# Performance work log

Hardware: AMD Instinct MI355X
Metric: run time of the kernel (lower is better)

## Reference

```python
import jax, jax.numpy as jnp
import numpy as np

N = 100000       # nodes
E = 1600000      # edges
IN = 256         # in_channels
H = 64           # hidden_channels
OUT = 40         # out_channels
K = 3            # hops

def setup_inputs() -> dict:
    key = jax.random.key(0)
    ks = jax.random.split(key, 20)
    f = lambda k, s: jax.random.normal(k, s, dtype=jnp.float32) * 0.05
    return {
        'x': f(ks[0], (N, IN)),
        'edge_index': jax.random.randint(ks[1], (2, E), 0, N),
        'W_in': f(ks[2], (H, IN)), 'b_in': f(ks[3], (H,)),
        'sg_W': f(ks[4], (K, H, H)), 'sg_b': f(ks[5], (K, H)),
        'in_proj_W': f(ks[6], (3 * H, H)), 'in_proj_b': f(ks[7], (3 * H,)),
        'out_W': f(ks[8], (H, H)), 'out_b': f(ks[9], (H,)),
        'ff_W1': f(ks[10], (2 * H, H)), 'ff_b1': f(ks[11], (2 * H,)),
        'ff_W2': f(ks[12], (H, 2 * H)), 'ff_b2': f(ks[13], (H,)),
        'ln1_w': jnp.ones((H,), jnp.float32), 'ln1_b': jnp.zeros((H,), jnp.float32),
        'ln2_w': jnp.ones((H,), jnp.float32), 'ln2_b': jnp.zeros((H,), jnp.float32),
        'cls_W': f(ks[14], (OUT, H)), 'cls_b': f(ks[15], (OUT,)),
    }

def _ln(x, w, b, eps=1e-5):
    m = x.mean(-1, keepdims=True)
    v = ((x - m) ** 2).mean(-1, keepdims=True)
    return (x - m) * jax.lax.rsqrt(v + eps) * w + b

def reference(x, edge_index, W_in, b_in, sg_W, sg_b, in_proj_W, in_proj_b,
              out_W, out_b, ff_W1, ff_b1, ff_W2, ff_b2,
              ln1_w, ln1_b, ln2_w, ln2_b, cls_W, cls_b):
    # --- gcn_norm with self loops (SGConv default) ---
    loop = jnp.arange(N)
    src = jnp.concatenate([edge_index[0], loop])
    dst = jnp.concatenate([edge_index[1], loop])
    deg = jax.ops.segment_sum(jnp.ones(src.shape[0], x.dtype), dst, num_segments=N)
    dinv = jnp.where(deg > 0, jax.lax.rsqrt(deg), 0.0)
    norm = dinv[src] * dinv[dst]  # [E+N]

    def prop(h):  # one symmetric-normalized propagation: S @ h
        return jax.ops.segment_sum(h[src] * norm[:, None], dst, num_segments=N)

    h0 = jax.nn.relu(x @ W_in.T + b_in)  # [N, H]
    # SGConv with K=hop recomputes S^hop h0; equivalently propagate iteratively
    tokens = [h0]
    p = h0
    for k in range(K):
        p = prop(p)
        tokens.append(jax.nn.relu(p @ sg_W[k].T + sg_b[k]))
    seq = jnp.stack(tokens, axis=1)  # [N, K+1, H]

    # --- TransformerEncoderLayer (nhead=1, post-norm, gelu), eval mode ---
    qkv = seq @ in_proj_W.T + in_proj_b
    q, kk, v = jnp.split(qkv, 3, axis=-1)
    scores = jnp.einsum('nsh,nth->nst', q, kk) / jnp.sqrt(jnp.asarray(H, seq.dtype))
    a = jnp.einsum('nst,nth->nsh', jax.nn.softmax(scores, axis=-1), v)
    a = a @ out_W.T + out_b
    seq = _ln(seq + a, ln1_w, ln1_b)
    ff = jax.nn.gelu(seq @ ff_W1.T + ff_b1, approximate=False) @ ff_W2.T + ff_b2
    seq = _ln(seq + ff, ln2_w, ln2_b)

    h = seq.mean(axis=1)  # [N, H]
    return h @ cls_W.T + cls_b  # [N, OUT]
```

## Files before the change

### kernel.cpp

```cpp
#include <hip/hip_runtime.h>
#include <hip/hip_bf16.h>
#include <math.h>

#define NN 100000
#define EE 1600000
#define OUTC 40
#define NB 391
#define NG 6250
#define CAP 64
#define NBIN 391
#define BCAP 6144

#define WP_WIN 0
#define WP_SG  16896
#define WP_QKV 30720
#define WP_WO  44544
#define WP_W1  49152
#define WP_W2  58368
#define WP_WC  67072
#define WP_TOT 70528

typedef __hip_bfloat16 bf16;
typedef __attribute__((ext_vector_type(8))) short bf16x8;
typedef __attribute__((ext_vector_type(4))) float f32x4;

__device__ __forceinline__ unsigned short f2us(float f){
  bf16 b = __float2bfloat16(f);
  unsigned short u; __builtin_memcpy(&u, &b, 2); return u;
}
__device__ __forceinline__ float us2f(unsigned short u){
  union{unsigned x; float f;} c; c.x = ((unsigned)u)<<16; return c.f;
}
__device__ __forceinline__ float lo_f(unsigned u){ union{unsigned x;float f;}c; c.x = u<<16; return c.f; }
__device__ __forceinline__ float hi_f(unsigned u){ union{unsigned x;float f;}c; c.x = u & 0xffff0000u; return c.f; }

__device__ __forceinline__ float gelu_f(float v){
  float ax = fabsf(v);
  float t  = __builtin_amdgcn_rcpf(fmaf(0.3275911f, ax, 1.0f));
  float p  = fmaf(t, 1.061405429f, -1.453152027f);
  p = fmaf(t, p, 1.421413741f);
  p = fmaf(t, p, -0.284496736f);
  p = fmaf(t, p, 0.254829592f);
  p = p * t;
  float ex = __expf(-ax*ax);
  float er = fmaf(-p, ex, 1.0f);
  er = copysignf(er, v);
  return 0.5f * v * (1.0f + er);
}

__global__ void k_wprep(const float* __restrict__ Win, const float* __restrict__ sgW,
                        const float* __restrict__ Wqkv, const float* __restrict__ Wo,
                        const float* __restrict__ W1, const float* __restrict__ W2,
                        const float* __restrict__ Wc, unsigned short* __restrict__ wp){
  for (int idx = blockIdx.x*blockDim.x + threadIdx.x; idx < WP_TOT;
       idx += gridDim.x*blockDim.x){
    float v; int o;
    if (idx < WP_SG){ o = idx; int r=o/264, c=o-r*264; v = (c<256)? Win[r*256+c] : 0.f; }
    else if (idx < WP_QKV){ o = idx-WP_SG; int h=o/4608, rem=o-h*4608, r=rem/72, c=rem-r*72;
      v=(c<64)? sgW[h*4096+r*64+c] : 0.f; }
    else if (idx < WP_WO){ o = idx-WP_QKV; int r=o/72, c=o-r*72; v=(c<64)? Wqkv[r*64+c]:0.f; }
    else if (idx < WP_W1){ o = idx-WP_WO; int r=o/72, c=o-r*72; v=(c<64)? Wo[r*64+c]:0.f; }
    else if (idx < WP_W2){ o = idx-WP_W1; int r=o/72, c=o-r*72; v=(c<64)? W1[r*64+c]:0.f; }
    else if (idx < WP_WC){ o = idx-WP_W2; int r=o/136, c=o-r*136; v=(c<128)? W2[r*128+c]:0.f; }
    else { o = idx-WP_WC; int r=o/72, c=o-r*72; v=(r<OUTC && c<64)? Wc[r*64+c]:0.f; }
    wp[idx] = f2us(v);
  }
}

__global__ void k_zero(int* p, int n){
  int i = blockIdx.x*blockDim.x + threadIdx.x;
  if (i < n) p[i] = 0;
}

__global__ void __launch_bounds__(256) k_bin(const int* __restrict__ ei,
    int* __restrict__ binFill, int2* __restrict__ binned){
  __shared__ int hist[NBIN], sbase[NBIN], loc[NBIN];
  const int tid = threadIdx.x;
  const int CH = (EE + gridDim.x - 1) / gridDim.x;
  const int e0 = blockIdx.x * CH;
  const int e1 = min(e0 + CH, EE);
  for (int i = tid; i < NBIN; i += 256){ hist[i] = 0; loc[i] = 0; }
  __syncthreads();
  for (int e = e0 + tid; e < e1; e += 256)
    atomicAdd(&hist[ei[EE + e] >> 8], 1);
  __syncthreads();
  for (int i = tid; i < NBIN; i += 256)
    sbase[i] = atomicAdd(&binFill[i], hist[i]);
  __syncthreads();
  for (int e = e0 + tid; e < e1; e += 256){
    int d = ei[EE + e];
    int s = ei[e];
    int b = d >> 8;
    int p = sbase[b] + atomicAdd(&loc[b], 1);
    if (p < BCAP) binned[(size_t)b*BCAP + p] = make_int2(s, d);
  }
}
__global__ void __launch_bounds__(256) k_bucket(const int* __restrict__ binFill,
    const int2* __restrict__ binned, int* __restrict__ srcb,
    int* __restrict__ cnt, float* __restrict__ dinv){
  __shared__ int lcnt[256];
  const int b = blockIdx.x, tid = threadIdx.x;
  lcnt[tid] = 0;
  __syncthreads();
  int m = binFill[b]; if (m > BCAP) m = BCAP;
  const int2* seg = binned + (size_t)b*BCAP;
  for (int e = tid; e < m; e += 256){
    int2 sd = seg[e];
    int dl = sd.y & 255;
    int p = atomicAdd(&lcnt[dl], 1);
    if (p < CAP) srcb[((size_t)(b << 8) + dl)*CAP + p] = sd.x;
  }
  __syncthreads();
  int d = (b << 8) + tid;
  if (d < NN){
    int c = lcnt[tid];
    dinv[d] = rsqrtf((float)c + 1.0f);
    cnt[d] = min(c, CAP);
  }
}

__global__ void __launch_bounds__(256) k_gather(const int* __restrict__ cnt,
    const int* __restrict__ srcb, const float* __restrict__ dinv,
    const unsigned short* __restrict__ prev, unsigned short* __restrict__ cur){
  int wid = (blockIdx.x*256 + threadIdx.x) >> 6;
  if (wid >= NN) return;
  const int lane = threadIdx.x & 63;
  const int grp = lane >> 4, cl = lane & 15;
  const int n = wid;
  const int deg = cnt[n];
  const int* bk = srcb + (size_t)n*CAP;
  const float dn = dinv[n];
  float a0=0.f, a1=0.f, a2=0.f, a3=0.f;
  int base = 0;
  if (8 <= deg){
    int s0 = bk[grp], s1 = bk[4+grp];
    float w0 = dinv[s0]*dn, w1 = dinv[s1]*dn;
    uint2 r0 = *(const uint2*)(prev + ((size_t)s0 << 6) + (cl << 2));
    uint2 r1 = *(const uint2*)(prev + ((size_t)s1 << 6) + (cl << 2));
    base = 8;
    for (; base + 8 <= deg; base += 8){
      int t0 = bk[base + grp], t1 = bk[base + 4 + grp];
      float x0 = dinv[t0]*dn, x1 = dinv[t1]*dn;
      uint2 q0 = *(const uint2*)(prev + ((size_t)t0 << 6) + (cl << 2));
      uint2 q1 = *(const uint2*)(prev + ((size_t)t1 << 6) + (cl << 2));
      a0 += lo_f(r0.x)*w0; a1 += hi_f(r0.x)*w0;
      a2 += lo_f(r0.y)*w0; a3 += hi_f(r0.y)*w0;
      a0 += lo_f(r1.x)*w1; a1 += hi_f(r1.x)*w1;
      a2 += lo_f(r1.y)*w1; a3 += hi_f(r1.y)*w1;
      s0 = t0; s1 = t1; w0 = x0; w1 = x1; r0 = q0; r1 = q1;
    }
    a0 += lo_f(r0.x)*w0; a1 += hi_f(r0.x)*w0;
    a2 += lo_f(r0.y)*w0; a3 += hi_f(r0.y)*w0;
    a0 += lo_f(r1.x)*w1; a1 += hi_f(r1.x)*w1;
    a2 += lo_f(r1.y)*w1; a3 += hi_f(r1.y)*w1;
  }
  for (; base < deg; base += 4){
    int idx = base + grp;
    int s = 0; float w = 0.f;
    if (idx < deg){ s = bk[idx]; w = dinv[s]*dn; }
    uint2 r0 = *(const uint2*)(prev + ((size_t)s << 6) + (cl << 2));
    a0 += lo_f(r0.x)*w; a1 += hi_f(r0.x)*w;
    a2 += lo_f(r0.y)*w; a3 += hi_f(r0.y)*w;
  }
  a0 += __shfl_xor(a0,16); a0 += __shfl_xor(a0,32);
  a1 += __shfl_xor(a1,16); a1 += __shfl_xor(a1,32);
  a2 += __shfl_xor(a2,16); a2 += __shfl_xor(a2,32);
  a3 += __shfl_xor(a3,16); a3 += __shfl_xor(a3,32);
  if (lane < 16){
    float d2 = dn*dn;
    uint2 sr = *(const uint2*)(prev + ((size_t)n << 6) + (cl << 2));
    a0 += lo_f(sr.x)*d2; a1 += hi_f(sr.x)*d2;
    a2 += lo_f(sr.y)*d2; a3 += hi_f(sr.y)*d2;
    unsigned p0 = (unsigned)f2us(a0) | ((unsigned)f2us(a1) << 16);
    unsigned p1 = (unsigned)f2us(a2) | ((unsigned)f2us(a3) << 16);
    *(uint2*)(cur + ((size_t)n << 6) + (cl << 2)) = make_uint2(p0, p1);
  }
}

__global__ void __launch_bounds__(256) k_h0(const float* __restrict__ x,
    const unsigned short* __restrict__ wp, const float* __restrict__ bin,
    unsigned short* __restrict__ tokB, unsigned short* __restrict__ p0){
  __shared__ __align__(16) unsigned short Xs[64*264];
  __shared__ __align__(16) unsigned short Ws[64*264];
  __shared__ float bs[64];
  const int tid = threadIdx.x;
  {
    const uint4* src = (const uint4*)(wp + WP_WIN);
    for (int idx = tid; idx < 2112; idx += 256) ((uint4*)Ws)[idx] = src[idx];
  }
  const int n0 = blockIdx.x * 64;
  for (int idx = tid; idx < 4096; idx += 256){
    int r = idx >> 6, c0 = (idx & 63) * 4;
    int n = n0 + r; if (n >= NN) n = NN-1;
    float4 v = *(const float4*)(x + (size_t)n*256 + c0);
    unsigned short* d = &Xs[r*264 + c0];
    d[0]=f2us(v.x); d[1]=f2us(v.y); d[2]=f2us(v.z); d[3]=f2us(v.w);
  }
  if (tid < 64) bs[tid] = bin[tid];
  __syncthreads();
  const int w = tid >> 6, lane = tid & 63, quad = lane >> 4, c = lane & 15;
  f32x4 acc[4] = {{0,0,0,0},{0,0,0,0},{0,0,0,0},{0,0,0,0}};
  #pragma unroll
  for (int ks = 0; ks < 8; ++ks){
    int k0 = ks*32 + quad*8;
    bf16x8 a = *(const bf16x8*)&Xs[(w*16 + c)*264 + k0];
    #pragma unroll
    for (int nt = 0; nt < 4; ++nt){
      bf16x8 b = *(const bf16x8*)&Ws[(nt*16 + c)*264 + k0];
      acc[nt] = __builtin_amdgcn_mfma_f32_16x16x32_bf16(a, b, acc[nt], 0,0,0);
    }
  }
  __syncthreads();
  #pragma unroll
  for (int nt = 0; nt < 4; ++nt){
    int col = nt*16 + c;
    float bb = bs[col];
    #pragma unroll
    for (int rg = 0; rg < 4; ++rg){
      int rloc = w*16 + quad*4 + rg;
      Xs[rloc*72 + col] = f2us(fmaxf(acc[nt][rg] + bb, 0.f));
    }
  }
  __syncthreads();
  for (int idx = tid; idx < 512; idx += 256){
    int r = idx >> 3, ch = idx & 7;
    int n = n0 + r;
    if (n < NN){
      uint4 v = *(const uint4*)&Xs[r*72 + ch*8];
      *(uint4*)(tokB + (size_t)n*64 + ch*8) = v;
      *(uint4*)(p0   + (size_t)n*64 + ch*8) = v;
    }
  }
}

__global__ void __launch_bounds__(256) k_token(const unsigned short* __restrict__ cur,
    const unsigned short* __restrict__ wsg, const float* __restrict__ sgb,
    unsigned short* __restrict__ tok){
  __shared__ __align__(16) unsigned short Xs[64*72];
  __shared__ __align__(16) unsigned short Ws[64*72];
  __shared__ float bs[64];
  const int tid = threadIdx.x;
  {
    const uint4* src = (const uint4*)wsg;
    for (int idx = tid; idx < 576; idx += 256) ((uint4*)Ws)[idx] = src[idx];
  }
  if (tid < 64) bs[tid] = sgb[tid];
  const int n0 = blockIdx.x*64;
  for (int idx = tid; idx < 512; idx += 256){
    int r = idx >> 3, ch = idx & 7;
    int n = n0 + r; if (n >= NN) n = NN-1;
    *(uint4*)&Xs[r*72 + ch*8] = *(const uint4*)(cur + (size_t)n*64 + ch*8);
  }
  __syncthreads();
  const int w = tid >> 6, lane = tid & 63, quad = lane >> 4, c = lane & 15;
  f32x4 acc[4] = {{0,0,0,0},{0,0,0,0},{0,0,0,0},{0,0,0,0}};
  #pragma unroll
  for (int ks = 0; ks < 2; ++ks){
    int k0 = ks*32 + quad*8;
    bf16x8 a = *(const bf16x8*)&Xs[(w*16 + c)*72 + k0];
    #pragma unroll
    for (int nt = 0; nt < 4; ++nt){
      bf16x8 b = *(const bf16x8*)&Ws[(nt*16 + c)*72 + k0];
      acc[nt] = __builtin_amdgcn_mfma_f32_16x16x32_bf16(a, b, acc[nt], 0,0,0);
    }
  }
  __syncthreads();
  #pragma unroll
  for (int nt = 0; nt < 4; ++nt){
    int col = nt*16 + c;
    float bb = bs[col];
    #pragma unroll
    for (int rg = 0; rg < 4; ++rg){
      int rloc = w*16 + quad*4 + rg;
      Xs[rloc*72 + col] = f2us(fmaxf(acc[nt][rg] + bb, 0.f));
    }
  }
  __syncthreads();
  for (int idx = tid; idx < 512; idx += 256){
    int r = idx >> 3, ch = idx & 7;
    int n = n0 + r;
    if (n < NN)
      *(uint4*)(tok + (size_t)n*64 + ch*8) = *(const uint4*)&Xs[r*72 + ch*8];
  }
}

__global__ void __launch_bounds__(256) k_attn(unsigned short* __restrict__ tokB,
    const unsigned short* __restrict__ wp, const float* __restrict__ bqkv,
    const float* __restrict__ bo, const float* __restrict__ ln1w,
    const float* __restrict__ ln1b){
  __shared__ __align__(16) unsigned short Xs[64*72];
  __shared__ float bq[192], bos[64], l1w[64], l1b[64];
  const int tid = threadIdx.x;
  if (tid < 192) bq[tid] = bqkv[tid];
  if (tid < 64){ bos[tid]=bo[tid]; l1w[tid]=ln1w[tid]; l1b[tid]=ln1b[tid]; }
  const int w = tid >> 6, lane = tid & 63, quad = lane >> 4, c = lane & 15;
  const int rw = w*16;
  const unsigned short* Wq  = wp + WP_QKV;
  const unsigned short* Wos = wp + WP_WO;
  for (int g = blockIdx.x; g < NG; g += gridDim.x){
    __syncthreads();
    for (int idx = tid; idx < 512; idx += 256){
      int r = idx >> 3, ch = idx & 7;
      int t = r & 3, n = g*16 + (r >> 2);
      *(uint4*)&Xs[r*72 + ch*8] = *(const uint4*)(tokB + ((size_t)t*NN + n)*64 + ch*8);
    }
    __syncthreads();
    bf16x8 a0 = *(const bf16x8*)&Xs[(rw+c)*72 + quad*8];
    bf16x8 a1 = *(const bf16x8*)&Xs[(rw+c)*72 + 32 + quad*8];
    float resv[4][4];
    #pragma unroll
    for (int nt = 0; nt < 4; ++nt){
      #pragma unroll
      for (int rg = 0; rg < 4; ++rg)
        resv[nt][rg] = us2f(Xs[(rw + quad*4 + rg)*72 + nt*16 + c]);
    }
    f32x4 qk[12];
    #pragma unroll
    for (int nt = 0; nt < 12; ++nt){
      f32x4 acc = {0,0,0,0};
      bf16x8 b0 = *(const bf16x8*)&Wq[(nt*16+c)*72 + quad*8];
      bf16x8 b1 = *(const bf16x8*)&Wq[(nt*16+c)*72 + 32 + quad*8];
      acc = __builtin_amdgcn_mfma_f32_16x16x32_bf16(a0, b0, acc, 0,0,0);
      acc = __builtin_amdgcn_mfma_f32_16x16x32_bf16(a1, b1, acc, 0,0,0);
      float bb = bq[nt*16 + c];
      acc[0]+=bb; acc[1]+=bb; acc[2]+=bb; acc[3]+=bb;
      qk[nt] = acc;
    }
    float sc[4][4];
    #pragma unroll
    for (int s = 0; s < 4; ++s){
      #pragma unroll
      for (int t = 0; t < 4; ++t){
        float p = qk[0][s]*qk[4][t] + qk[1][s]*qk[5][t]
                + qk[2][s]*qk[6][t] + qk[3][s]*qk[7][t];
        p += __shfl_xor(p, 1); p += __shfl_xor(p, 2);
        p += __shfl_xor(p, 4); p += __shfl_xor(p, 8);
        sc[s][t] = p * 0.125f;
      }
    }
    float pm[4][4];
    #pragma unroll
    for (int s = 0; s < 4; ++s){
      float m = fmaxf(fmaxf(sc[s][0],sc[s][1]), fmaxf(sc[s][2],sc[s][3]));
      float e0=__expf(sc[s][0]-m), e1=__expf(sc[s][1]-m);
      float e2=__expf(sc[s][2]-m), e3=__expf(sc[s][3]-m);
      float inv = 1.f/(e0+e1+e2+e3);
      pm[s][0]=e0*inv; pm[s][1]=e1*inv; pm[s][2]=e2*inv; pm[s][3]=e3*inv;
    }
    #pragma unroll
    for (int tile = 0; tile < 4; ++tile){
      #pragma unroll
      for (int s = 0; s < 4; ++s){
        float av = pm[s][0]*qk[8+tile][0] + pm[s][1]*qk[8+tile][1]
                 + pm[s][2]*qk[8+tile][2] + pm[s][3]*qk[8+tile][3];
        Xs[(rw + quad*4 + s)*72 + tile*16 + c] = f2us(av);
      }
    }
    bf16x8 p0 = *(const bf16x8*)&Xs[(rw+c)*72 + quad*8];
    bf16x8 p1 = *(const bf16x8*)&Xs[(rw+c)*72 + 32 + quad*8];
    f32x4 ov[4];
    #pragma unroll
    for (int nt = 0; nt < 4; ++nt){
      f32x4 acc = {0,0,0,0};
      bf16x8 b0 = *(const bf16x8*)&Wos[(nt*16+c)*72 + quad*8];
      bf16x8 b1 = *(const bf16x8*)&Wos[(nt*16+c)*72 + 32 + quad*8];
      acc = __builtin_amdgcn_mfma_f32_16x16x32_bf16(p0, b0, acc, 0,0,0);
      acc = __builtin_amdgcn_mfma_f32_16x16x32_bf16(p1, b1, acc, 0,0,0);
      ov[nt] = acc;
    }
    float r4[4][4];
    #pragma unroll
    for (int nt = 0; nt < 4; ++nt){
      int col = nt*16 + c;
      float bb = bos[col];
      #pragma unroll
      for (int rg = 0; rg < 4; ++rg)
        r4[nt][rg] = ov[nt][rg] + bb + resv[nt][rg];
    }
    #pragma unroll
    for (int rg = 0; rg < 4; ++rg){
      float sm = r4[0][rg]+r4[1][rg]+r4[2][rg]+r4[3][rg];
      sm += __shfl_xor(sm,1); sm += __shfl_xor(sm,2);
      sm += __shfl_xor(sm,4); sm += __shfl_xor(sm,8);
      float mean = sm * (1.f/64.f);
      float d0=r4[0][rg]-mean, d1=r4[1][rg]-mean, d2=r4[2][rg]-mean, d3=r4[3][rg]-mean;
      float vs = d0*d0+d1*d1+d2*d2+d3*d3;
      vs += __shfl_xor(vs,1); vs += __shfl_xor(vs,2);
      vs += __shfl_xor(vs,4); vs += __shfl_xor(vs,8);
      float rinv = rsqrtf(vs*(1.f/64.f) + 1e-5f);
      int row = rw + quad*4 + rg;
      #pragma unroll
      for (int nt = 0; nt < 4; ++nt){
        int col = nt*16 + c;
        Xs[row*72 + col] = f2us((r4[nt][rg] - mean) * rinv * l1w[col] + l1b[col]);
      }
    }
    __syncthreads();
    for (int idx = tid; idx < 512; idx += 256){
      int r = idx >> 3, ch = idx & 7;
      int t = r & 3, n = g*16 + (r >> 2);
      *(uint4*)(tokB + ((size_t)t*NN + n)*64 + ch*8) = *(const uint4*)&Xs[r*72 + ch*8];
    }
  }
}

__global__ void __launch_bounds__(256) k_ffn(const unsigned short* __restrict__ tokB,
    const unsigned short* __restrict__ wp,
    const float* __restrict__ b1, const float* __restrict__ b2,
    const float* __restrict__ ln2w, const float* __restrict__ ln2b,
    const float* __restrict__ bc, float* __restrict__ out){
  __shared__ __align__(16) unsigned short Xs[64*72];
  __shared__ __align__(16) unsigned short F1[64*136];
  __shared__ __align__(16) unsigned short hsH[16*72];
  __shared__ __align__(16) unsigned short hsL[16*72];
  __shared__ float b1s[128], b2s[64], l2w[64], l2b[64], bcs[40];
  const int tid = threadIdx.x;
  if (tid < 128) b1s[tid] = b1[tid];
  if (tid < 64){ b2s[tid]=b2[tid]; l2w[tid]=ln2w[tid]; l2b[tid]=ln2b[tid]; }
  if (tid < 40)  bcs[tid] = bc[tid];
  const int w = tid >> 6, lane = tid & 63, quad = lane >> 4, c = lane & 15;
  const int rw = w*16;
  const unsigned short* W1g = wp + WP_W1;
  const unsigned short* W2g = wp + WP_W2;
  const unsigned short* Wcg = wp + WP_WC;
  for (int g = blockIdx.x; g < NG; g += gridDim.x){
    __syncthreads();
    for (int idx = tid; idx < 512; idx += 256){
      int r = idx >> 3, ch = idx & 7;
      int t = r & 3, n = g*16 + (r >> 2);
      *(uint4*)&Xs[r*72 + ch*8] = *(const uint4*)(tokB + ((size_t)t*NN + n)*64 + ch*8);
    }
    __syncthreads();
    bf16x8 a0 = *(const bf16x8*)&Xs[(rw+c)*72 + quad*8];
    bf16x8 a1 = *(const bf16x8*)&Xs[(rw+c)*72 + 32 + quad*8];
    #pragma unroll
    for (int nt = 0; nt < 8; ++nt){
      f32x4 acc = {0,0,0,0};
      bf16x8 b0 = *(const bf16x8*)&W1g[(nt*16+c)*72 + quad*8];
      bf16x8 b1v = *(const bf16x8*)&W1g[(nt*16+c)*72 + 32 + quad*8];
      acc = __builtin_amdgcn_mfma_f32_16x16x32_bf16(a0, b0, acc, 0,0,0);
      acc = __builtin_amdgcn_mfma_f32_16x16x32_bf16(a1, b1v, acc, 0,0,0);
      float bb = b1s[nt*16 + c];
      #pragma unroll
      for (int rg = 0; rg < 4; ++rg){
        float v = acc[rg] + bb;
        F1[(rw + quad*4 + rg)*136 + nt*16 + c] = f2us(gelu_f(v));
      }
    }
    bf16x8 fa[4];
    #pragma unroll
    for (int ks = 0; ks < 4; ++ks)
      fa[ks] = *(const bf16x8*)&F1[(rw+c)*136 + ks*32 + quad*8];
    f32x4 ov[4];
    #pragma unroll
    for (int nt = 0; nt < 4; ++nt){
      f32x4 acc = {0,0,0,0};
      #pragma unroll
      for (int ks = 0; ks < 4; ++ks){
        bf16x8 b = *(const bf16x8*)&W2g[(nt*16+c)*136 + ks*32 + quad*8];
        acc = __builtin_amdgcn_mfma_f32_16x16x32_bf16(fa[ks], b, acc, 0,0,0);
      }
      ov[nt] = acc;
    }
    float r4[4][4];
    #pragma unroll
    for (int nt = 0; nt < 4; ++nt){
      int col = nt*16 + c;
      float bb = b2s[col];
      #pragma unroll
      for (int rg = 0; rg < 4; ++rg){
        float seqv = us2f(Xs[(rw + quad*4 + rg)*72 + col]);
        r4[nt][rg] = ov[nt][rg] + bb + seqv;
      }
    }
    float hval[4] = {0.f, 0.f, 0.f, 0.f};
    #pragma unroll
    for (int rg = 0; rg < 4; ++rg){
      float sm = r4[0][rg]+r4[1][rg]+r4[2][rg]+r4[3][rg];
      sm += __shfl_xor(sm,1); sm += __shfl_xor(sm,2);
      sm += __shfl_xor(sm,4); sm += __shfl_xor(sm,8);
      float mean = sm * (1.f/64.f);
      float d0=r4[0][rg]-mean, d1=r4[1][rg]-mean, d2=r4[2][rg]-mean, d3=r4[3][rg]-mean;
      float vs = d0*d0+d1*d1+d2*d2+d3*d3;
      vs += __shfl_xor(vs,1); vs += __shfl_xor(vs,2);
      vs += __shfl_xor(vs,4); vs += __shfl_xor(vs,8);
      float rinv = rsqrtf(vs*(1.f/64.f) + 1e-5f);
      #pragma unroll
      for (int nt = 0; nt < 4; ++nt){
        int col = nt*16 + c;
        hval[nt] += (r4[nt][rg] - mean) * rinv * l2w[col] + l2b[col];
      }
    }
    #pragma unroll
    for (int nt = 0; nt < 4; ++nt){
      float hv = hval[nt] * 0.25f;
      unsigned short hh = f2us(hv);
      float lo = hv - us2f(hh);
      hsH[(w*4 + quad)*72 + nt*16 + c] = hh;
      hsL[(w*4 + quad)*72 + nt*16 + c] = f2us(lo);
    }
    __syncthreads();
    if (w < 3){
      bf16x8 hA0 = *(const bf16x8*)&hsH[c*72 + quad*8];
      bf16x8 hA1 = *(const bf16x8*)&hsH[c*72 + 32 + quad*8];
      bf16x8 lA0 = *(const bf16x8*)&hsL[c*72 + quad*8];
      bf16x8 lA1 = *(const bf16x8*)&hsL[c*72 + 32 + quad*8];
      bf16x8 wB0 = *(const bf16x8*)&Wcg[(w*16 + c)*72 + quad*8];
      bf16x8 wB1 = *(const bf16x8*)&Wcg[(w*16 + c)*72 + 32 + quad*8];
      f32x4 acc = {0,0,0,0};
      acc = __builtin_amdgcn_mfma_f32_16x16x32_bf16(hA0, wB0, acc, 0,0,0);
      acc = __builtin_amdgcn_mfma_f32_16x16x32_bf16(hA1, wB1, acc, 0,0,0);
      acc = __builtin_amdgcn_mfma_f32_16x16x32_bf16(lA0, wB0, acc, 0,0,0);
      acc = __builtin_amdgcn_mfma_f32_16x16x32_bf16(lA1, wB1, acc, 0,0,0);
      int o = w*16 + c;
      if (o < OUTC){
        float bb = bcs[o];
        #pragma unroll
        for (int rg = 0; rg < 4; ++rg)
          out[(size_t)(g*16 + quad*4 + rg)*OUTC + o] = acc[rg] + bb;
      }
    }
  }
}

extern "C" void kernel_launch(void* const* d_in, const int* in_sizes, int n_in,
                              void* d_out, int out_size, void* d_ws, size_t ws_size,
                              hipStream_t stream) {
  const float* x    = (const float*)d_in[0];
  const int*   ei   = (const int*  )d_in[1];
  const float* Win  = (const float*)d_in[2];
  const float* bin  = (const float*)d_in[3];
  const float* sgW  = (const float*)d_in[4];
  const float* sgb  = (const float*)d_in[5];
  const float* Wqkv = (const float*)d_in[6];
  const float* bqkv = (const float*)d_in[7];
  const float* Wo   = (const float*)d_in[8];
  const float* bo   = (const float*)d_in[9];
  const float* W1   = (const float*)d_in[10];
  const float* b1   = (const float*)d_in[11];
  const float* W2   = (const float*)d_in[12];
  const float* b2   = (const float*)d_in[13];
  const float* ln1w = (const float*)d_in[14];
  const float* ln1b = (const float*)d_in[15];
  const float* ln2w = (const float*)d_in[16];
  const float* ln2b = (const float*)d_in[17];
  const float* Wc   = (const float*)d_in[18];
  const float* bc   = (const float*)d_in[19];

  char* ws = (char*)d_ws;
  float*          dinv = (float*)(ws);
  int*            cnt  = (int*  )(ws + 400128);
  unsigned short* wp   = (unsigned short*)(ws + 800256);
  unsigned short* tokB = (unsigned short*)(ws + 941568);
  unsigned short* pb0  = (unsigned short*)(ws + 52141696);
  unsigned short* pb1  = (unsigned short*)(ws + 64941824);
  int2* binned  = (int2*)pb0;
  int*  binFill = (int*)tokB;
  int*  srcb    = (int*)(tokB + (size_t)2*NN*64);

  k_wprep<<<128, 256, 0, stream>>>(Win, sgW, Wqkv, Wo, W1, W2, Wc, wp);

  k_zero  <<<2, 256, 0, stream>>>(binFill, NBIN);
  k_bin   <<<512, 256, 0, stream>>>(ei, binFill, binned);
  k_bucket<<<NBIN, 256, 0, stream>>>(binFill, binned, srcb, cnt, dinv);

  const int GB = (NN + 63) / 64;
  const int GG = (NN*64 + 255) / 256;
  k_h0<<<GB, 256, 0, stream>>>(x, wp, bin, tokB, pb0);

  k_gather<<<GG, 256, 0, stream>>>(cnt, srcb, dinv, pb0, pb1);
  k_token <<<GB, 256, 0, stream>>>(pb1, wp + WP_SG,        sgb,       tokB + (size_t)1*NN*64);
  k_gather<<<GG, 256, 0, stream>>>(cnt, srcb, dinv, pb1, pb0);
  k_gather<<<GG, 256, 0, stream>>>(cnt, srcb, dinv, pb0, pb1);
  k_token <<<GB, 256, 0, stream>>>(pb0, wp + WP_SG + 4608, sgb + 64,  tokB + (size_t)2*NN*64);
  k_token <<<GB, 256, 0, stream>>>(pb1, wp + WP_SG + 9216, sgb + 128, tokB + (size_t)3*NN*64);

  k_attn<<<2048, 256, 0, stream>>>(tokB, wp, bqkv, bo, ln1w, ln1b);
  k_ffn <<<2048, 256, 0, stream>>>(tokB, wp, b1, b2, ln2w, ln2b, bc, (float*)d_out);
}
```

Before: 608.4 us.

## Fuse attention and FFN kernels; widen gather loads to 16 bytes per lane

Merges the attention and FFN kernels into one kernel that keeps the LN1 output in shared memory instead of writing it to tokB and reading it back, which removes one global round trip of the token tensor. The attention output now goes to the F1 buffer so Xs can still supply the residual. Separately, the gather kernel now has each lane load 8 bf16 values (uint4) across 8 lanes per row, processing 8 or 16 edges per step. The cost is a larger shared-memory footprint per block, more registers in the fused kernel, and more shuffle steps in the gather reduction.

```diff
diff --git a/kernel.cpp b/kernel.cpp
--- a/kernel.cpp
+++ b/kernel.cpp
@@ -119,61 +119,66 @@
   }
 }
 
+#define GACC(r, wt) \
+  a0 += lo_f((r).x)*(wt); a1 += hi_f((r).x)*(wt); \
+  a2 += lo_f((r).y)*(wt); a3 += hi_f((r).y)*(wt); \
+  a4 += lo_f((r).z)*(wt); a5 += hi_f((r).z)*(wt); \
+  a6 += lo_f((r).w)*(wt); a7 += hi_f((r).w)*(wt);
+
 __global__ void __launch_bounds__(256) k_gather(const int* __restrict__ cnt,
     const int* __restrict__ srcb, const float* __restrict__ dinv,
     const unsigned short* __restrict__ prev, unsigned short* __restrict__ cur){
   int wid = (blockIdx.x*256 + threadIdx.x) >> 6;
   if (wid >= NN) return;
   const int lane = threadIdx.x & 63;
-  const int grp = lane >> 4, cl = lane & 15;
+  const int grp = lane >> 3, cl = lane & 7;
   const int n = wid;
   const int deg = cnt[n];
   const int* bk = srcb + (size_t)n*CAP;
   const float dn = dinv[n];
-  float a0=0.f, a1=0.f, a2=0.f, a3=0.f;
+  float a0=0,a1=0,a2=0,a3=0,a4=0,a5=0,a6=0,a7=0;
   int base = 0;
-  if (8 <= deg){
-    int s0 = bk[grp], s1 = bk[4+grp];
+  if (16 <= deg){
+    int s0 = bk[grp], s1 = bk[8 + grp];
     float w0 = dinv[s0]*dn, w1 = dinv[s1]*dn;
-    uint2 r0 = *(const uint2*)(prev + ((size_t)s0 << 6) + (cl << 2));
-    uint2 r1 = *(const uint2*)(prev + ((size_t)s1 << 6) + (cl << 2));
-    base = 8;
-    for (; base + 8 <= deg; base += 8){
-      int t0 = bk[base + grp], t1 = bk[base + 4 + grp];
+    uint4 r0 = *(const uint4*)(prev + ((size_t)s0 << 6) + (cl << 3));
+    uint4 r1 = *(const uint4*)(prev + ((size_t)s1 << 6) + (cl << 3));
+    base = 16;
+    for (; base + 16 <= deg; base += 16){
+      int t0 = bk[base + grp], t1 = bk[base + 8 + grp];
       float x0 = dinv[t0]*dn, x1 = dinv[t1]*dn;
-      uint2 q0 = *(const uint2*)(prev + ((size_t)t0 << 6) + (cl << 2));
-      uint2 q1 = *(const uint2*)(prev + ((size_t)t1 << 6) + (cl << 2));
-      a0 += lo_f(r0.x)*w0; a1 += hi_f(r0.x)*w0;
-      a2 += lo_f(r0.y)*w0; a3 += hi_f(r0.y)*w0;
-      a0 += lo_f(r1.x)*w1; a1 += hi_f(r1.x)*w1;
-      a2 += lo_f(r1.y)*w1; a3 += hi_f(r1.y)*w1;
+      uint4 q0 = *(const uint4*)(prev + ((size_t)t0 << 6) + (cl << 3));
+      uint4 q1 = *(const uint4*)(prev + ((size_t)t1 << 6) + (cl << 3));
+      GACC(r0, w0); GACC(r1, w1);
       s0 = t0; s1 = t1; w0 = x0; w1 = x1; r0 = q0; r1 = q1;
     }
-    a0 += lo_f(r0.x)*w0; a1 += hi_f(r0.x)*w0;
-    a2 += lo_f(r0.y)*w0; a3 += hi_f(r0.y)*w0;
-    a0 += lo_f(r1.x)*w1; a1 += hi_f(r1.x)*w1;
-    a2 += lo_f(r1.y)*w1; a3 += hi_f(r1.y)*w1;
-  }
-  for (; base < deg; base += 4){
+    GACC(r0, w0); GACC(r1, w1);
+  }
+  for (; base < deg; base += 8){
     int idx = base + grp;
-    int s = 0; float w = 0.f;
-    if (idx < deg){ s = bk[idx]; w = dinv[s]*dn; }
-    uint2 r0 = *(const uint2*)(prev + ((size_t)s << 6) + (cl << 2));
-    a0 += lo_f(r0.x)*w; a1 += hi_f(r0.x)*w;
-    a2 += lo_f(r0.y)*w; a3 += hi_f(r0.y)*w;
-  }
-  a0 += __shfl_xor(a0,16); a0 += __shfl_xor(a0,32);
-  a1 += __shfl_xor(a1,16); a1 += __shfl_xor(a1,32);
-  a2 += __shfl_xor(a2,16); a2 += __shfl_xor(a2,32);
-  a3 += __shfl_xor(a3,16); a3 += __shfl_xor(a3,32);
-  if (lane < 16){
+    int s = 0; float wv = 0.f;
+    if (idx < deg){ s = bk[idx]; wv = dinv[s]*dn; }
+    uint4 r = *(const uint4*)(prev + ((size_t)s << 6) + (cl << 3));
+    GACC(r, wv);
+  }
+  a0 += __shfl_xor(a0,8); a0 += __shfl_xor(a0,16); a0 += __shfl_xor(a0,32);
+  a1 += __shfl_xor(a1,8); a1 += __shfl_xor(a1,16); a1 += __shfl_xor(a1,32);
+  a2 += __shfl_xor(a2,8); a2 += __shfl_xor(a2,16); a2 += __shfl_xor(a2,32);
+  a3 += __shfl_xor(a3,8); a3 += __shfl_xor(a3,16); a3 += __shfl_xor(a3,32);
+  a4 += __shfl_xor(a4,8); a4 += __shfl_xor(a4,16); a4 += __shfl_xor(a4,32);
+  a5 += __shfl_xor(a5,8); a5 += __shfl_xor(a5,16); a5 += __shfl_xor(a5,32);
+  a6 += __shfl_xor(a6,8); a6 += __shfl_xor(a6,16); a6 += __shfl_xor(a6,32);
+  a7 += __shfl_xor(a7,8); a7 += __shfl_xor(a7,16); a7 += __shfl_xor(a7,32);
+  if (lane < 8){
     float d2 = dn*dn;
-    uint2 sr = *(const uint2*)(prev + ((size_t)n << 6) + (cl << 2));
-    a0 += lo_f(sr.x)*d2; a1 += hi_f(sr.x)*d2;
-    a2 += lo_f(sr.y)*d2; a3 += hi_f(sr.y)*d2;
-    unsigned p0 = (unsigned)f2us(a0) | ((unsigned)f2us(a1) << 16);
-    unsigned p1 = (unsigned)f2us(a2) | ((unsigned)f2us(a3) << 16);
-    *(uint2*)(cur + ((size_t)n << 6) + (cl << 2)) = make_uint2(p0, p1);
+    uint4 sr = *(const uint4*)(prev + ((size_t)n << 6) + (cl << 3));
+    GACC(sr, d2);
+    uint4 pk;
+    pk.x = (unsigned)f2us(a0) | ((unsigned)f2us(a1) << 16);
+    pk.y = (unsigned)f2us(a2) | ((unsigned)f2us(a3) << 16);
+    pk.z = (unsigned)f2us(a4) | ((unsigned)f2us(a5) << 16);
+    pk.w = (unsigned)f2us(a6) | ((unsigned)f2us(a7) << 16);
+    *(uint4*)(cur + ((size_t)n << 6) + (cl << 3)) = pk;
   }
 }
 
@@ -284,19 +289,32 @@
   }
 }
 
-__global__ void __launch_bounds__(256) k_attn(unsigned short* __restrict__ tokB,
+__global__ void __launch_bounds__(256) k_attn_ffn(const unsigned short* __restrict__ tokB,
     const unsigned short* __restrict__ wp, const float* __restrict__ bqkv,
     const float* __restrict__ bo, const float* __restrict__ ln1w,
-    const float* __restrict__ ln1b){
+    const float* __restrict__ ln1b,
+    const float* __restrict__ b1, const float* __restrict__ b2,
+    const float* __restrict__ ln2w, const float* __restrict__ ln2b,
+    const float* __restrict__ bc, float* __restrict__ out){
   __shared__ __align__(16) unsigned short Xs[64*72];
+  __shared__ __align__(16) unsigned short F1[64*136];
+  __shared__ __align__(16) unsigned short hsH[16*72];
+  __shared__ __align__(16) unsigned short hsL[16*72];
   __shared__ float bq[192], bos[64], l1w[64], l1b[64];
+  __shared__ float b1s[128], b2s[64], l2w[64], l2b[64], bcs[40];
   const int tid = threadIdx.x;
   if (tid < 192) bq[tid] = bqkv[tid];
-  if (tid < 64){ bos[tid]=bo[tid]; l1w[tid]=ln1w[tid]; l1b[tid]=ln1b[tid]; }
+  if (tid < 128) b1s[tid] = b1[tid];
+  if (tid < 64){ bos[tid]=bo[tid]; l1w[tid]=ln1w[tid]; l1b[tid]=ln1b[tid];
+                 b2s[tid]=b2[tid]; l2w[tid]=ln2w[tid]; l2b[tid]=ln2b[tid]; }
+  if (tid < 40)  bcs[tid] = bc[tid];
   const int w = tid >> 6, lane = tid & 63, quad = lane >> 4, c = lane & 15;
   const int rw = w*16;
   const unsigned short* Wq  = wp + WP_QKV;
   const unsigned short* Wos = wp + WP_WO;
+  const unsigned short* W1g = wp + WP_W1;
+  const unsigned short* W2g = wp + WP_W2;
+  const unsigned short* Wcg = wp + WP_WC;
   for (int g = blockIdx.x; g < NG; g += gridDim.x){
     __syncthreads();
     for (int idx = tid; idx < 512; idx += 256){
@@ -307,21 +325,14 @@
     __syncthreads();
     bf16x8 a0 = *(const bf16x8*)&Xs[(rw+c)*72 + quad*8];
     bf16x8 a1 = *(const bf16x8*)&Xs[(rw+c)*72 + 32 + quad*8];
-    float resv[4][4];
-    #pragma unroll
-    for (int nt = 0; nt < 4; ++nt){
-      #pragma unroll
-      for (int rg = 0; rg < 4; ++rg)
-        resv[nt][rg] = us2f(Xs[(rw + quad*4 + rg)*72 + nt*16 + c]);
-    }
     f32x4 qk[12];
     #pragma unroll
     for (int nt = 0; nt < 12; ++nt){
       f32x4 acc = {0,0,0,0};
       bf16x8 b0 = *(const bf16x8*)&Wq[(nt*16+c)*72 + quad*8];
-      bf16x8 b1 = *(const bf16x8*)&Wq[(nt*16+c)*72 + 32 + quad*8];
+      bf16x8 b1v = *(const bf16x8*)&Wq[(nt*16+c)*72 + 32 + quad*8];
       acc = __builtin_amdgcn_mfma_f32_16x16x32_bf16(a0, b0, acc, 0,0,0);
-      acc = __builtin_amdgcn_mfma_f32_16x16x32_bf16(a1, b1, acc, 0,0,0);
+      acc = __builtin_amdgcn_mfma_f32_16x16x32_bf16(a1, b1v, acc, 0,0,0);
       float bb = bq[nt*16 + c];
       acc[0]+=bb; acc[1]+=bb; acc[2]+=bb; acc[3]+=bb;
       qk[nt] = acc;
@@ -353,19 +364,19 @@
       for (int s = 0; s < 4; ++s){
         float av = pm[s][0]*qk[8+tile][0] + pm[s][1]*qk[8+tile][1]
                  + pm[s][2]*qk[8+tile][2] + pm[s][3]*qk[8+tile][3];
-        Xs[(rw + quad*4 + s)*72 + tile*16 + c] = f2us(av);
-      }
-    }
-    bf16x8 p0 = *(const bf16x8*)&Xs[(rw+c)*72 + quad*8];
-    bf16x8 p1 = *(const bf16x8*)&Xs[(rw+c)*72 + 32 + quad*8];
+        F1[(rw + quad*4 + s)*72 + tile*16 + c] = f2us(av);
+      }
+    }
+    bf16x8 p0 = *(const bf16x8*)&F1[(rw+c)*72 + quad*8];
+    bf16x8 p1 = *(const bf16x8*)&F1[(rw+c)*72 + 32 + quad*8];
     f32x4 ov[4];
     #pragma unroll
     for (int nt = 0; nt < 4; ++nt){
       f32x4 acc = {0,0,0,0};
       bf16x8 b0 = *(const bf16x8*)&Wos[(nt*16+c)*72 + quad*8];
-      bf16x8 b1 = *(const bf16x8*)&Wos[(nt*16+c)*72 + 32 + quad*8];
+      bf16x8 b1v = *(const bf16x8*)&Wos[(nt*16+c)*72 + 32 + quad*8];
       acc = __builtin_amdgcn_mfma_f32_16x16x32_bf16(p0, b0, acc, 0,0,0);
-      acc = __builtin_amdgcn_mfma_f32_16x16x32_bf16(p1, b1, acc, 0,0,0);
+      acc = __builtin_amdgcn_mfma_f32_16x16x32_bf16(p1, b1v, acc, 0,0,0);
       ov[nt] = acc;
     }
     float r4[4][4];
@@ -374,8 +385,10 @@
       int col = nt*16 + c;
       float bb = bos[col];
       #pragma unroll
-      for (int rg = 0; rg < 4; ++rg)
-        r4[nt][rg] = ov[nt][rg] + bb + resv[nt][rg];
+      for (int rg = 0; rg < 4; ++rg){
+        float seqv = us2f(Xs[(rw + quad*4 + rg)*72 + col]);
+        r4[nt][rg] = ov[nt][rg] + bb + seqv;
+      }
     }
     #pragma unroll
     for (int rg = 0; rg < 4; ++rg){
@@ -395,51 +408,15 @@
         Xs[row*72 + col] = f2us((r4[nt][rg] - mean) * rinv * l1w[col] + l1b[col]);
       }
     }
-    __syncthreads();
-    for (int idx = tid; idx < 512; idx += 256){
-      int r = idx >> 3, ch = idx & 7;
-      int t = r & 3, n = g*16 + (r >> 2);
-      *(uint4*)(tokB + ((size_t)t*NN + n)*64 + ch*8) = *(const uint4*)&Xs[r*72 + ch*8];
-    }
-  }
-}
-
-__global__ void __launch_bounds__(256) k_ffn(const unsigned short* __restrict__ tokB,
-    const unsigned short* __restrict__ wp,
-    const float* __restrict__ b1, const float* __restrict__ b2,
-    const float* __restrict__ ln2w, const float* __restrict__ ln2b,
-    const float* __restrict__ bc, float* __restrict__ out){
-  __shared__ __align__(16) unsigned short Xs[64*72];
-  __shared__ __align__(16) unsigned short F1[64*136];
-  __shared__ __align__(16) unsigned short hsH[16*72];
-  __shared__ __align__(16) unsigned short hsL[16*72];
-  __shared__ float b1s[128], b2s[64], l2w[64], l2b[64], bcs[40];
-  const int tid = threadIdx.x;
-  if (tid < 128) b1s[tid] = b1[tid];
-  if (tid < 64){ b2s[tid]=b2[tid]; l2w[tid]=ln2w[tid]; l2b[tid]=ln2b[tid]; }
-  if (tid < 40)  bcs[tid] = bc[tid];
-  const int w = tid >> 6, lane = tid & 63, quad = lane >> 4, c = lane & 15;
-  const int rw = w*16;
-  const unsigned short* W1g = wp + WP_W1;
-  const unsigned short* W2g = wp + WP_W2;
-  const unsigned short* Wcg = wp + WP_WC;
-  for (int g = blockIdx.x; g < NG; g += gridDim.x){
-    __syncthreads();
-    for (int idx = tid; idx < 512; idx += 256){
-      int r = idx >> 3, ch = idx & 7;
-      int t = r & 3, n = g*16 + (r >> 2);
-      *(uint4*)&Xs[r*72 + ch*8] = *(const uint4*)(tokB + ((size_t)t*NN + n)*64 + ch*8);
-    }
-    __syncthreads();
-    bf16x8 a0 = *(const bf16x8*)&Xs[(rw+c)*72 + quad*8];
-    bf16x8 a1 = *(const bf16x8*)&Xs[(rw+c)*72 + 32 + quad*8];
+    bf16x8 fA0 = *(const bf16x8*)&Xs[(rw+c)*72 + quad*8];
+    bf16x8 fA1 = *(const bf16x8*)&Xs[(rw+c)*72 + 32 + quad*8];
     #pragma unroll
     for (int nt = 0; nt < 8; ++nt){
       f32x4 acc = {0,0,0,0};
       bf16x8 b0 = *(const bf16x8*)&W1g[(nt*16+c)*72 + quad*8];
       bf16x8 b1v = *(const bf16x8*)&W1g[(nt*16+c)*72 + 32 + quad*8];
-      acc = __builtin_amdgcn_mfma_f32_16x16x32_bf16(a0, b0, acc, 0,0,0);
-      acc = __builtin_amdgcn_mfma_f32_16x16x32_bf16(a1, b1v, acc, 0,0,0);
+      acc = __builtin_amdgcn_mfma_f32_16x16x32_bf16(fA0, b0, acc, 0,0,0);
+      acc = __builtin_amdgcn_mfma_f32_16x16x32_bf16(fA1, b1v, acc, 0,0,0);
       float bb = b1s[nt*16 + c];
       #pragma unroll
       for (int rg = 0; rg < 4; ++rg){
@@ -451,7 +428,6 @@
     #pragma unroll
     for (int ks = 0; ks < 4; ++ks)
       fa[ks] = *(const bf16x8*)&F1[(rw+c)*136 + ks*32 + quad*8];
-    f32x4 ov[4];
     #pragma unroll
     for (int nt = 0; nt < 4; ++nt){
       f32x4 acc = {0,0,0,0};
@@ -462,7 +438,6 @@
       }
       ov[nt] = acc;
     }
-    float r4[4][4];
     #pragma unroll
     for (int nt = 0; nt < 4; ++nt){
       int col = nt*16 + c;
@@ -575,6 +550,6 @@
   k_token <<<GB, 256, 0, stream>>>(pb0, wp + WP_SG + 4608, sgb + 64,  tokB + (size_t)2*NN*64);
   k_token <<<GB, 256, 0, stream>>>(pb1, wp + WP_SG + 9216, sgb + 128, tokB + (size_t)3*NN*64);
 
-  k_attn<<<2048, 256, 0, stream>>>(tokB, wp, bqkv, bo, ln1w, ln1b);
-  k_ffn <<<2048, 256, 0, stream>>>(tokB, wp, b1, b2, ln2w, ln2b, bc, (float*)d_out);
-}
+  k_attn_ffn<<<2048, 256, 0, stream>>>(tokB, wp, bqkv, bo, ln1w, ln1b,
+                                       b1, b2, ln2w, ln2b, bc, (float*)d_out);
+}
```

Result: slower. 711.5 us (+17.0%).
